# Performance work log

Hardware: AMD Instinct MI355X
Metric: run time of the kernel (lower is better)

Reference implementation:

```python
import jax, jax.numpy as jnp
import numpy as np

EPS = 1e-5
N_HEAD = 16
N_LOCAL = 4
HEAD_DIM = 128
DIM = 2048
B, S = 2, 2048


def rms_norm(x, w):
    # torch nn.RMSNorm: x / sqrt(mean(x^2, -1) + eps) * w
    var = jnp.mean(jnp.square(x), axis=-1, keepdims=True)
    return x * jax.lax.rsqrt(var + EPS) * w


def apply_rotary_emb(x, freqs_cis):
    # x: [B, S, H, D]; freqs_cis: [S, D//2, 2]
    xs = x.reshape(*x.shape[:-1], -1, 2)  # [B,S,H,D/2,2]
    fc = freqs_cis[None, :, None, :, :]   # [1,S,1,D/2,2]
    xr, xi = xs[..., 0], xs[..., 1]
    cr, ci = fc[..., 0], fc[..., 1]
    out = jnp.stack([xr * cr - xi * ci, xi * cr + xr * ci], axis=-1)
    return out.reshape(x.shape)


def setup_inputs() -> dict:
    key = jax.random.key(0)
    ks = jax.random.split(key, 6)
    x = jax.random.normal(ks[0], (B, S, DIM), dtype=jnp.float32)
    # rotary cos/sin table
    inv_freq = 1.0 / (10000.0 ** (np.arange(0, HEAD_DIM, 2, dtype=np.float32) / HEAD_DIM))
    t = np.arange(S, dtype=np.float32)
    ang = np.outer(t, inv_freq)  # [S, D/2]
    freqs_cis = jnp.asarray(np.stack([np.cos(ang), np.sin(ang)], axis=-1))  # [S,D/2,2]
    mask = jnp.tril(jnp.ones((S, S), dtype=bool))[None, None]  # [1,1,S,S]
    wqkv = jax.random.normal(ks[1], ((N_HEAD + 2 * N_LOCAL) * HEAD_DIM, DIM), dtype=jnp.float32) * (DIM ** -0.5)
    wo = jax.random.normal(ks[2], (DIM, N_HEAD * HEAD_DIM), dtype=jnp.float32) * ((N_HEAD * HEAD_DIM) ** -0.5)
    q_norm_w = jnp.ones((HEAD_DIM,), dtype=jnp.float32)
    k_norm_w = jnp.ones((HEAD_DIM,), dtype=jnp.float32)
    return {"x": x, "freqs_cis": freqs_cis, "mask": mask, "wqkv": wqkv, "wo": wo,
            "q_norm_w": q_norm_w, "k_norm_w": k_norm_w}


def reference(x, freqs_cis, mask, wqkv, wo, q_norm_w, k_norm_w):
    bsz, seqlen, _ = x.shape
    q_size = N_HEAD * HEAD_DIM
    kv_size = N_LOCAL * HEAD_DIM
    qkv = jnp.einsum('bsd,ed->bse', x, wqkv)  # fused QKV projection
    q = qkv[..., :q_size].reshape(bsz, seqlen, N_HEAD, HEAD_DIM)
    k = qkv[..., q_size:q_size + kv_size].reshape(bsz, seqlen, N_LOCAL, HEAD_DIM)
    v = qkv[..., q_size + kv_size:].reshape(bsz, seqlen, N_LOCAL, HEAD_DIM)
    q = rms_norm(q, q_norm_w)
    k = rms_norm(k, k_norm_w)
    q = apply_rotary_emb(q, freqs_cis)
    k = apply_rotary_emb(k, freqs_cis)
    # GQA: group queries over shared k/v heads instead of repeat_interleave
    g = N_HEAD // N_LOCAL
    qg = q.reshape(bsz, seqlen, N_LOCAL, g, HEAD_DIM)
    scale = HEAD_DIM ** -0.5
    scores = jnp.einsum('bqhgd,bkhd->bhgqk', qg, k) * scale  # [B,nl,g,S,S]
    scores = jnp.where(mask[:, :, None], scores, jnp.finfo(scores.dtype).min)
    attn = jax.nn.softmax(scores, axis=-1)
    y = jnp.einsum('bhgqk,bkhd->bqhgd', attn, v)  # [B,S,nl,g,D]
    y = y.reshape(bsz, seqlen, q_size)
    return jnp.einsum('bse,de->bsd', y, wo)
```

## Files before the change

kernel.cpp:

```cpp
#include <hip/hip_runtime.h>
#include <stdint.h>

#define S_LEN 2048
#define DIM   2048
#define NH    16
#define NKV   4
#define HD    128
#define QKV_E 3072

typedef unsigned short u16;
typedef __attribute__((ext_vector_type(8))) short short8;
typedef __attribute__((ext_vector_type(4))) float floatx4;

__device__ __forceinline__ u16 f2bf(float f) {
  unsigned u = __float_as_uint(f);
  u = u + 0x7fffu + ((u >> 16) & 1u);
  return (u16)(u >> 16);
}
__device__ __forceinline__ float bf2f(u16 b) {
  return __uint_as_float(((unsigned)b) << 16);
}

__global__ __launch_bounds__(256) void cast_bf16_k(const float* __restrict__ in,
                                                   u16* __restrict__ out, int n4) {
  int i = blockIdx.x * blockDim.x + threadIdx.x;
  int stride = gridDim.x * blockDim.x;
  for (; i < n4; i += stride) {
    float4 v = ((const float4*)in)[i];
    ushort4 o;
    o.x = f2bf(v.x); o.y = f2bf(v.y); o.z = f2bf(v.z); o.w = f2bf(v.w);
    ((ushort4*)out)[i] = o;
  }
}

#define GT 128
#define GBK 32

__device__ __forceinline__ void gload16(const void* g, void* l) {
  __builtin_amdgcn_global_load_lds((const __attribute__((address_space(1))) void*)g,
                                   (__attribute__((address_space(3))) void*)l, 16, 0, 0);
}

__global__ __launch_bounds__(256) void gemm_bt(const u16* __restrict__ A,
                                               const u16* __restrict__ B,
                                               float* __restrict__ C,
                                               u16* __restrict__ Cb,
                                               int M, int N, int K, int obf16) {
  __shared__ u16 As[GT * GBK];
  __shared__ u16 Bs[GT * GBK];
  const int tid  = threadIdx.x;
  const int wid  = tid >> 6;
  const int lane = tid & 63;
  const int m0 = blockIdx.y * GT;
  const int n0 = blockIdx.x * GT;
  const int wr = wid >> 1, wc = wid & 1;

  floatx4 acc[4][4] = {};

  const int srow   = lane >> 2;
  const int schunk = (lane & 3) * 8;
  const int fr = lane & 15;
  const int kc = (lane >> 4) * 8;

  for (int k0 = 0; k0 < K; k0 += GBK) {
#pragma unroll
    for (int i = 0; i < 2; ++i) {
      int r = i * 64 + wid * 16 + srow;
      gload16(A + (size_t)(m0 + r) * K + k0 + schunk, As + (i * 64 + wid * 16) * GBK);
      gload16(B + (size_t)(n0 + r) * K + k0 + schunk, Bs + (i * 64 + wid * 16) * GBK);
    }
    __syncthreads();

    short8 af[4], bf[4];
#pragma unroll
    for (int m = 0; m < 4; ++m)
      af[m] = *(const short8*)(As + (wr * 64 + m * 16 + fr) * GBK + kc);
#pragma unroll
    for (int n = 0; n < 4; ++n)
      bf[n] = *(const short8*)(Bs + (wc * 64 + n * 16 + fr) * GBK + kc);
#pragma unroll
    for (int m = 0; m < 4; ++m)
#pragma unroll
      for (int n = 0; n < 4; ++n)
        acc[m][n] = __builtin_amdgcn_mfma_f32_16x16x32_bf16(af[m], bf[n], acc[m][n], 0, 0, 0);
    __syncthreads();
  }

#pragma unroll
  for (int m = 0; m < 4; ++m)
#pragma unroll
    for (int n = 0; n < 4; ++n) {
      int row = m0 + wr * 64 + m * 16 + (lane >> 4) * 4;
      int col = n0 + wc * 64 + n * 16 + (lane & 15);
      if (obf16) {
        u16* cp = Cb + (size_t)row * N + col;
#pragma unroll
        for (int r = 0; r < 4; ++r) cp[(size_t)r * N] = f2bf(acc[m][n][r]);
      } else {
        float* cp = C + (size_t)row * N + col;
#pragma unroll
        for (int r = 0; r < 4; ++r) cp[(size_t)r * N] = acc[m][n][r];
      }
    }
}

__global__ __launch_bounds__(256) void normrope(const u16* __restrict__ qkv,
                                                const float* __restrict__ freqs,
                                                const float* __restrict__ qw,
                                                const float* __restrict__ kw,
                                                u16* __restrict__ Qb,
                                                u16* __restrict__ Kb,
                                                u16* __restrict__ Vt) {
  int row  = blockIdx.x * 4 + (threadIdx.x >> 6);
  int lane = threadIdx.x & 63;
  int bs = row / 24, h = row % 24;
  int b = bs >> 11, s = bs & (S_LEN - 1);
  const u16* src = qkv + (size_t)bs * QKV_E + h * HD;
  ushort2 xr = *(const ushort2*)(src + 2 * lane);
  float x0 = bf2f(xr.x), x1 = bf2f(xr.y);

  float ss = x0 * x0 + x1 * x1;
#pragma unroll
  for (int off = 32; off; off >>= 1) ss += __shfl_xor(ss, off);
  float rn = rsqrtf(ss * (1.0f / 128.0f) + 1e-5f);

  const float scale = 0.08838834764831845f;
  if (h < 20) {
    const float* w = (h < 16) ? qw : kw;
    float y0 = x0 * rn * w[2 * lane];
    float y1 = x1 * rn * w[2 * lane + 1];
    float2 f = *(const float2*)(freqs + (size_t)s * 128 + 2 * lane);
    float r0 = y0 * f.x - y1 * f.y;
    float r1 = y1 * f.x + y0 * f.y;
    ushort2 o;
    if (h < 16) { o.x = f2bf(r0 * scale); o.y = f2bf(r1 * scale); }
    else        { o.x = f2bf(r0);         o.y = f2bf(r1); }
    u16* dst = (h < 16) ? (Qb + ((size_t)(b * NH  + h)      * S_LEN + s) * HD)
                        : (Kb + ((size_t)(b * NKV + h - 16) * S_LEN + s) * HD);
    *(ushort2*)(dst + 2 * lane) = o;
  } else {
    u16* dst = Vt + (size_t)(b * NKV + (h - 20)) * HD * S_LEN;
    dst[(size_t)(2 * lane)     * S_LEN + s] = f2bf(x0);
    dst[(size_t)(2 * lane + 1) * S_LEN + s] = f2bf(x1);
  }
}

#define KT 64

__global__ __launch_bounds__(256) void attn_mfma(const u16* __restrict__ Qb,
                                                 const u16* __restrict__ Kb,
                                                 const u16* __restrict__ Vt,
                                                 u16* __restrict__ Yb) {
  __shared__ u16 Ks[KT * HD];
  __shared__ u16 VtS[HD * KT];
  __shared__ unsigned PsT[4][32 * 18];

  const int wid  = threadIdx.x >> 6;
  const int lane = threadIdx.x & 63;
  const int gg   = lane >> 4;
  const int c16  = lane & 15;
  const int b = blockIdx.z, h = blockIdx.y, bx = blockIdx.x;
  const int hv = h >> 2;

  const u16* Qp = Qb + ((size_t)(b * NH  + h)  * S_LEN) * HD;
  const u16* Kp = Kb + ((size_t)(b * NKV + hv) * S_LEN) * HD;
  const u16* Vp = Vt + ((size_t)(b * NKV + hv) * HD) * S_LEN;

  short8 onesf;
#pragma unroll
  for (int i = 0; i < 8; ++i) onesf[i] = (short)0x3F80;

  for (int pass = 0; pass < 2; ++pass) {
    const int qt  = pass ? (31 - bx) : bx;
    const int q0  = qt * 64;
    const int qw0 = q0 + wid * 16;

    short8 qf[4];
    {
      const u16* qrow = Qp + (size_t)(qw0 + c16) * HD + gg * 8;
#pragma unroll
      for (int ds = 0; ds < 4; ++ds) qf[ds] = *(const short8*)(qrow + ds * 32);
    }

    floatx4 Oacc[8] = {};
    floatx4 Lacc = {};

    for (int k0 = 0; k0 < q0 + 64; k0 += KT) {
#pragma unroll
      for (int i = 0; i < 4; ++i) {
        int rbase = wid * 16 + i * 4;
        int r = rbase + gg;
        int cb = c16 * 16;
        gload16((const char*)Kp + (size_t)(k0 + r) * 256 + (cb ^ ((r & 7) << 4)),
                (char*)Ks + rbase * 256);
      }
#pragma unroll
      for (int i = 0; i < 4; ++i) {
        int rbase = wid * 32 + i * 8;
        int r = rbase + (lane >> 3);
        int cb = (lane & 7) * 16;
        gload16((const char*)Vp + (size_t)r * (S_LEN * 2) + (size_t)k0 * 2 + (cb ^ ((r & 7) << 4)),
                (char*)VtS + rbase * 128);
      }
      __syncthreads();

      if (k0 <= qw0 + 15) {
        floatx4 st[4] = {};
#pragma unroll
        for (int kt = 0; kt < 4; ++kt) {
          int krow = kt * 16 + c16;
          const char* kbase = (const char*)Ks + krow * 256;
          int swz = (krow & 7) << 4;
#pragma unroll
          for (int ds = 0; ds < 4; ++ds) {
            short8 kf = *(const short8*)(kbase + ((ds * 64 + gg * 16) ^ swz));
            st[kt] = __builtin_amdgcn_mfma_f32_16x16x32_bf16(kf, qf[ds], st[kt], 0, 0, 0);
          }
        }

        const int q = qw0 + c16;
        const bool full = (k0 + 63 <= qw0);
#pragma unroll
        for (int kt = 0; kt < 4; ++kt) {
          float p[4];
#pragma unroll
          for (int r = 0; r < 4; ++r) {
            int k = k0 + kt * 16 + gg * 4 + r;
            float e = __expf(st[kt][r]);
            p[r] = (full || k <= q) ? e : 0.f;
          }
          unsigned w0, w1;
          asm("v_cvt_pk_bf16_f32 %0, %1, %2" : "=v"(w0) : "v"(p[0]), "v"(p[1]));
          asm("v_cvt_pk_bf16_f32 %0, %1, %2" : "=v"(w1) : "v"(p[2]), "v"(p[3]));
          unsigned* pp = &PsT[wid][(kt * 8 + gg * 2) * 18 + c16];
          pp[0]  = w0;
          pp[18] = w1;
        }

        short8 pfr[2];
#pragma unroll
        for (int ktp = 0; ktp < 2; ++ktp) {
          const unsigned* pp = &PsT[wid][(ktp * 16 + gg * 4) * 18 + c16];
          unsigned u[4];
          u[0] = pp[0]; u[1] = pp[18]; u[2] = pp[36]; u[3] = pp[54];
          pfr[ktp] = *(const short8*)u;
        }

#pragma unroll
        for (int ktp = 0; ktp < 2; ++ktp)
          Lacc = __builtin_amdgcn_mfma_f32_16x16x32_bf16(pfr[ktp], onesf, Lacc, 0, 0, 0);

#pragma unroll
        for (int dt = 0; dt < 8; ++dt) {
          int vrow = dt * 16 + c16;
          int swzv = (vrow & 7) << 4;
#pragma unroll
          for (int ktp = 0; ktp < 2; ++ktp) {
            short8 vf = *(const short8*)((const char*)VtS + vrow * 128 + ((ktp * 64 + gg * 16) ^ swzv));
            Oacc[dt] = __builtin_amdgcn_mfma_f32_16x16x32_bf16(pfr[ktp], vf, Oacc[dt], 0, 0, 0);
          }
        }
      }
      __syncthreads();
    }

    float linv[4];
#pragma unroll
    for (int r = 0; r < 4; ++r) linv[r] = 1.0f / Lacc[r];
#pragma unroll
    for (int dt = 0; dt < 8; ++dt) {
      int d = dt * 16 + c16;
#pragma unroll
      for (int r = 0; r < 4; ++r) {
        int qg = qw0 + gg * 4 + r;
        Yb[((size_t)(b * S_LEN + qg)) * DIM + h * HD + d] = f2bf(Oacc[dt][r] * linv[r]);
      }
    }
  }
}

extern "C" void kernel_launch(void* const* d_in, const int* in_sizes, int n_in,
                              void* d_out, int out_size, void* d_ws, size_t ws_size,
                              hipStream_t stream) {
  const float* x     = (const float*)d_in[0];
  const float* freqs = (const float*)d_in[1];
  const float* wqkv  = (const float*)d_in[3];
  const float* wo    = (const float*)d_in[4];
  const float* qw    = (const float*)d_in[5];
  const float* kw    = (const float*)d_in[6];
  float* out = (float*)d_out;
  char* ws = (char*)d_ws;

  const int M = 2 * S_LEN;

  u16* xb    = (u16*)(ws);
  u16* wqkvb = (u16*)(ws + 16777216);
  u16* wob   = (u16*)(ws + 29360128);
  u16* qkvb  = (u16*)(ws + 37748736);
  u16* Qb    = (u16*)(ws + 62914560);
  u16* Kb    = (u16*)(ws + 79691776);
  u16* Vt    = (u16*)(ws + 83886080);
  u16* Yb    = (u16*)(ws + 88080384);

  cast_bf16_k<<<2048, 256, 0, stream>>>(x,    xb,    M * DIM / 4);
  cast_bf16_k<<<2048, 256, 0, stream>>>(wqkv, wqkvb, QKV_E * DIM / 4);
  cast_bf16_k<<<2048, 256, 0, stream>>>(wo,   wob,   DIM * DIM / 4);

  gemm_bt<<<dim3(QKV_E / GT, M / GT), 256, 0, stream>>>(xb, wqkvb, nullptr, qkvb,
                                                        M, QKV_E, DIM, 1);

  normrope<<<(M * 24) / 4, 256, 0, stream>>>(qkvb, freqs, qw, kw, Qb, Kb, Vt);

  attn_mfma<<<dim3(16, NH, 2), 256, 0, stream>>>(Qb, Kb, Vt, Yb);

  gemm_bt<<<dim3(DIM / GT, M / GT), 256, 0, stream>>>(Yb, wob, out, nullptr,
                                                      M, DIM, DIM, 0);
}
```

Baseline: 353.5 us.

## Replace GEMM with 256x256 double-buffered swizzled LDS pipeline and fuse casts

Replaces the 128x128, single-buffered GEMM with a 512-thread 256x256 tile kernel. It uses BK=64, double-buffered LDS with XOR swizzling, and staggered prefetch of half-tiles interleaved with MFMA phases, plus s_setprio around the compute. The three fp32-to-bf16 cast launches are merged into one kernel. The aim is to hide global load latency, cut LDS bank conflicts, and improve operand reuse per loaded byte. In exchange it uses 128KB of dynamic shared memory, which limits occupancy, and the larger tiles give fewer blocks: 96 for the QKV GEMM and 64 for the output projection, which may underfill the CUs.

Measured after the change: 363.1 us. 2.7% more time.

```diff
diff --git a/kernel.cpp b/kernel.cpp
--- a/kernel.cpp
+++ b/kernel.cpp
@@ -21,85 +21,145 @@
   return __uint_as_float(((unsigned)b) << 16);
 }
 
-__global__ __launch_bounds__(256) void cast_bf16_k(const float* __restrict__ in,
-                                                   u16* __restrict__ out, int n4) {
-  int i = blockIdx.x * blockDim.x + threadIdx.x;
-  int stride = gridDim.x * blockDim.x;
-  for (; i < n4; i += stride) {
-    float4 v = ((const float4*)in)[i];
-    ushort4 o;
-    o.x = f2bf(v.x); o.y = f2bf(v.y); o.z = f2bf(v.z); o.w = f2bf(v.w);
-    ((ushort4*)out)[i] = o;
-  }
-}
-
-#define GT 128
-#define GBK 32
-
 __device__ __forceinline__ void gload16(const void* g, void* l) {
   __builtin_amdgcn_global_load_lds((const __attribute__((address_space(1))) void*)g,
                                    (__attribute__((address_space(3))) void*)l, 16, 0, 0);
 }
 
-__global__ __launch_bounds__(256) void gemm_bt(const u16* __restrict__ A,
-                                               const u16* __restrict__ B,
-                                               float* __restrict__ C,
-                                               u16* __restrict__ Cb,
-                                               int M, int N, int K, int obf16) {
-  __shared__ u16 As[GT * GBK];
-  __shared__ u16 Bs[GT * GBK];
+__global__ __launch_bounds__(256) void cast3(const float* __restrict__ x,
+                                             const float* __restrict__ wq,
+                                             const float* __restrict__ wo,
+                                             u16* __restrict__ xb,
+                                             u16* __restrict__ wqb,
+                                             u16* __restrict__ wob) {
+  const int n1 = 2097152;
+  const int n2 = n1 + 1572864;
+  const int n3 = n2 + 1048576;
+  int i = blockIdx.x * 256 + threadIdx.x;
+  for (; i < n3; i += gridDim.x * 256) {
+    const float* s; u16* d; int j;
+    if (i < n1)      { s = x;  d = xb;  j = i; }
+    else if (i < n2) { s = wq; d = wqb; j = i - n1; }
+    else             { s = wo; d = wob; j = i - n2; }
+    float4 v = ((const float4*)s)[j];
+    ushort4 o;
+    o.x = f2bf(v.x); o.y = f2bf(v.y); o.z = f2bf(v.z); o.w = f2bf(v.w);
+    ((ushort4*)d)[j] = o;
+  }
+}
+
+
+#define FENCE() asm volatile("" ::: "memory")
+#define BARF()  do { FENCE(); __builtin_amdgcn_s_barrier(); FENCE(); } while (0)
+
+template <int OBF16>
+__global__ __launch_bounds__(512, 2) void gemm256(const u16* __restrict__ A,
+                                                  const u16* __restrict__ B,
+                                                  float* __restrict__ C,
+                                                  u16* __restrict__ Cb,
+                                                  int M, int N, int K) {
+  extern __shared__ char sm[];
   const int tid  = threadIdx.x;
   const int wid  = tid >> 6;
   const int lane = tid & 63;
-  const int m0 = blockIdx.y * GT;
-  const int n0 = blockIdx.x * GT;
-  const int wr = wid >> 1, wc = wid & 1;
-
-  floatx4 acc[4][4] = {};
-
-  const int srow   = lane >> 2;
-  const int schunk = (lane & 3) * 8;
-  const int fr = lane & 15;
-  const int kc = (lane >> 4) * 8;
-
-  for (int k0 = 0; k0 < K; k0 += GBK) {
+  const int gg   = lane >> 4;
+  const int c16  = lane & 15;
+  const int wm   = wid >> 2;
+  const int wn   = wid & 3;
+  const int m0 = blockIdx.y * 256;
+  const int n0 = blockIdx.x * 256;
+  const int NT = K >> 6;
+
+  floatx4 acc[8][4] = {};
+
+  auto stageA = [&](int kt, int h) {
 #pragma unroll
     for (int i = 0; i < 2; ++i) {
-      int r = i * 64 + wid * 16 + srow;
-      gload16(A + (size_t)(m0 + r) * K + k0 + schunk, As + (i * 64 + wid * 16) * GBK);
-      gload16(B + (size_t)(n0 + r) * K + k0 + schunk, Bs + (i * 64 + wid * 16) * GBK);
-    }
-    __syncthreads();
-
-    short8 af[4], bf[4];
-#pragma unroll
-    for (int m = 0; m < 4; ++m)
-      af[m] = *(const short8*)(As + (wr * 64 + m * 16 + fr) * GBK + kc);
-#pragma unroll
-    for (int n = 0; n < 4; ++n)
-      bf[n] = *(const short8*)(Bs + (wc * 64 + n * 16 + fr) * GBK + kc);
-#pragma unroll
-    for (int m = 0; m < 4; ++m)
-#pragma unroll
-      for (int n = 0; n < 4; ++n)
-        acc[m][n] = __builtin_amdgcn_mfma_f32_16x16x32_bf16(af[m], bf[n], acc[m][n], 0, 0, 0);
-    __syncthreads();
+      int lr = wid * 16 + i * 8 + (lane >> 3);
+      int sb = (lane & 7) * 16;
+      int grow = (lr >> 6) * 128 + h * 64 + (lr & 63);
+      const char* g = (const char*)(A + (size_t)(m0 + grow) * K + (size_t)kt * 64)
+                      + (sb ^ ((lr & 7) << 4));
+      gload16(g, sm + (kt & 1) * 32768 + h * 16384 + (wid * 16 + i * 8) * 128);
+    }
+  };
+  auto stageB = [&](int kt, int g) {
+#pragma unroll
+    for (int i = 0; i < 2; ++i) {
+      int lr = wid * 16 + i * 8 + (lane >> 3);
+      int sb = (lane & 7) * 16;
+      int grow = (lr >> 5) * 64 + g * 32 + (lr & 31);
+      const char* gp = (const char*)(B + (size_t)(n0 + grow) * K + (size_t)kt * 64)
+                       + (sb ^ ((lr & 7) << 4));
+      gload16(gp, sm + 65536 + (kt & 1) * 32768 + g * 16384 + (wid * 16 + i * 8) * 128);
+    }
+  };
+
+  stageA(0, 0); stageB(0, 0); stageA(0, 1); stageB(0, 1);
+  stageA(1, 0); stageB(1, 0);
+  asm volatile("s_waitcnt vmcnt(4)" ::: "memory");
+  BARF();
+
+#define GPHASE(MH, NG, STAGE_CODE)                                              \
+  do {                                                                          \
+    short8 af[4][2], bfv[2][2];                                                 \
+    const char* Abase = sm + buf * 32768 + (MH) * 16384;                        \
+    const char* Bbase = sm + 65536 + buf * 32768 + (NG) * 16384;                \
+    _Pragma("unroll") for (int mm = 0; mm < 4; ++mm) {                          \
+      int lr = wm * 64 + mm * 16 + c16;                                         \
+      _Pragma("unroll") for (int ks = 0; ks < 2; ++ks)                          \
+        af[mm][ks] = *(const short8*)(Abase + lr * 128 +                        \
+                        ((ks * 64 + gg * 16) ^ ((lr & 7) << 4)));               \
+    }                                                                           \
+    _Pragma("unroll") for (int nn = 0; nn < 2; ++nn) {                          \
+      int lr = wn * 32 + nn * 16 + c16;                                         \
+      _Pragma("unroll") for (int ks = 0; ks < 2; ++ks)                          \
+        bfv[nn][ks] = *(const short8*)(Bbase + lr * 128 +                       \
+                        ((ks * 64 + gg * 16) ^ ((lr & 7) << 4)));               \
+    }                                                                           \
+    STAGE_CODE;                                                                 \
+    BARF();                                                                     \
+    __builtin_amdgcn_s_setprio(1);                                              \
+    _Pragma("unroll") for (int mm = 0; mm < 4; ++mm)                            \
+      _Pragma("unroll") for (int nn = 0; nn < 2; ++nn) {                        \
+        acc[(MH)*4+mm][(NG)*2+nn] = __builtin_amdgcn_mfma_f32_16x16x32_bf16(    \
+            af[mm][0], bfv[nn][0], acc[(MH)*4+mm][(NG)*2+nn], 0, 0, 0);         \
+        acc[(MH)*4+mm][(NG)*2+nn] = __builtin_amdgcn_mfma_f32_16x16x32_bf16(    \
+            af[mm][1], bfv[nn][1], acc[(MH)*4+mm][(NG)*2+nn], 0, 0, 0);         \
+      }                                                                         \
+    __builtin_amdgcn_s_setprio(0);                                              \
+    FENCE();                                                                    \
+  } while (0)
+
+  for (int t = 0; t < NT; ++t) {
+    const int buf = t & 1;
+    GPHASE(0, 0, { if (t + 1 < NT) stageA(t + 1, 1); });
+    BARF();
+    GPHASE(0, 1, { if (t + 1 < NT) stageB(t + 1, 1); });
+    BARF();
+    GPHASE(1, 0, { if (t + 2 < NT) stageA(t + 2, 0); });
+    BARF();
+    GPHASE(1, 1, { if (t + 2 < NT) stageB(t + 2, 0); });
+    if (t + 2 < NT) asm volatile("s_waitcnt vmcnt(4)" ::: "memory");
+    else            asm volatile("s_waitcnt vmcnt(0)" ::: "memory");
+    BARF();
   }
-
-#pragma unroll
-  for (int m = 0; m < 4; ++m)
-#pragma unroll
-    for (int n = 0; n < 4; ++n) {
-      int row = m0 + wr * 64 + m * 16 + (lane >> 4) * 4;
-      int col = n0 + wc * 64 + n * 16 + (lane & 15);
-      if (obf16) {
+#undef GPHASE
+
+#pragma unroll
+  for (int mf = 0; mf < 8; ++mf)
+#pragma unroll
+    for (int nf = 0; nf < 4; ++nf) {
+      int row = m0 + wm * 128 + mf * 16 + gg * 4;
+      int col = n0 + wn * 64 + nf * 16 + c16;
+      if (OBF16) {
         u16* cp = Cb + (size_t)row * N + col;
 #pragma unroll
-        for (int r = 0; r < 4; ++r) cp[(size_t)r * N] = f2bf(acc[m][n][r]);
+        for (int r = 0; r < 4; ++r) cp[(size_t)r * N] = f2bf(acc[mf][nf][r]);
       } else {
         float* cp = C + (size_t)row * N + col;
 #pragma unroll
-        for (int r = 0; r < 4; ++r) cp[(size_t)r * N] = acc[m][n][r];
+        for (int r = 0; r < 4; ++r) cp[(size_t)r * N] = acc[mf][nf][r];
       }
     }
 }
@@ -302,17 +362,20 @@
   u16* Vt    = (u16*)(ws + 83886080);
   u16* Yb    = (u16*)(ws + 88080384);
 
-  cast_bf16_k<<<2048, 256, 0, stream>>>(x,    xb,    M * DIM / 4);
-  cast_bf16_k<<<2048, 256, 0, stream>>>(wqkv, wqkvb, QKV_E * DIM / 4);
-  cast_bf16_k<<<2048, 256, 0, stream>>>(wo,   wob,   DIM * DIM / 4);
-
-  gemm_bt<<<dim3(QKV_E / GT, M / GT), 256, 0, stream>>>(xb, wqkvb, nullptr, qkvb,
-                                                        M, QKV_E, DIM, 1);
+  hipFuncSetAttribute((const void*)gemm256<1>,
+                      hipFuncAttributeMaxDynamicSharedMemorySize, 131072);
+  hipFuncSetAttribute((const void*)gemm256<0>,
+                      hipFuncAttributeMaxDynamicSharedMemorySize, 131072);
+
+  cast3<<<2048, 256, 0, stream>>>(x, wqkv, wo, xb, wqkvb, wob);
+
+  gemm256<1><<<dim3(QKV_E / 256, M / 256), 512, 131072, stream>>>(
+      xb, wqkvb, nullptr, qkvb, M, QKV_E, DIM);
 
   normrope<<<(M * 24) / 4, 256, 0, stream>>>(qkvb, freqs, qw, kw, Qb, Kb, Vt);
 
   attn_mfma<<<dim3(16, NH, 2), 256, 0, stream>>>(Qb, Kb, Vt, Yb);
 
-  gemm_bt<<<dim3(DIM / GT, M / GT), 256, 0, stream>>>(Yb, wob, out, nullptr,
-                                                      M, DIM, DIM, 0);
-}
+  gemm256<0><<<dim3(DIM / 256, M / 256), 512, 131072, stream>>>(
+      Yb, wob, out, nullptr, M, DIM, DIM);
+}
```
